# Optimization experiments

Measured on AMD Instinct MI355X. Metric: run time of the kernel, lower is better.

## Reference

```python
import jax, jax.numpy as jnp
import numpy as np

NOISE_STD = 0.001


def setup_inputs() -> dict:
    key = jax.random.key(0)
    k1, k2, k3, k4 = jax.random.split(key, 4)
    B, T, NIN, NREC = 64, 2048, 64, 1024
    x = jax.random.normal(k1, (B, T, NIN), dtype=jnp.float32)
    W_ih = jax.random.normal(k2, (NREC, NIN), dtype=jnp.float32) / np.sqrt(NIN)
    W_hh = jax.random.normal(k3, (NREC, NREC), dtype=jnp.float32) / np.sqrt(NREC)
    noise = jax.random.normal(k4, (T, NREC), dtype=jnp.float32)
    return {"x": x, "W_ih": W_ih, "W_hh": W_hh, "noise": noise}


def reference(x, W_ih, W_hh, noise):
    # x: [B, T, n_in] -> scan over time (strict sequential dependency)
    B = x.shape[0]
    NREC = W_hh.shape[0]
    x_t = jnp.transpose(x, (1, 0, 2))            # [T, B, n_in]
    xproj = jnp.einsum('tbi,ri->tbr', x_t, W_ih)  # hoist input GEMM out of scan
    noise_scaled = noise * NOISE_STD              # [T, NREC], broadcast over batch
    h0 = jnp.zeros((B, NREC), dtype=x.dtype)

    def step(h_prev, inp):
        xp, n_t = inp
        h = xp + jnp.tanh(h_prev) @ W_hh.T + n_t[None, :]
        return h, h[-1]  # original appends h_t[-1] (last batch element)

    h_last, outs = jax.lax.scan(step, h0, (xproj, noise_scaled))
    output = outs.T  # stack -> [T, NREC], transpose(0,1) -> [NREC, T]
    return output, h_last
```

## Files before the change

kernel.cpp:

```cpp
#include <hip/hip_runtime.h>


#define TT    2048
#define BB    64
#define NIN   64
#define NRECN 1024
#define KTOT  1088
#define MT    32
#define NT    32
#define NGRP  2
#define WPG   32
#define NWG   (NGRP * WPG)
#define NOISE_STD 0.001f

typedef __attribute__((ext_vector_type(8))) short short8;
typedef __attribute__((ext_vector_type(4))) float f32x4;

__device__ __forceinline__ unsigned short f2bf(float f) {
  unsigned u = __float_as_uint(f);
  u += 0x7FFFu + ((u >> 16) & 1u);
  return (unsigned short)(u >> 16);
}
__device__ __forceinline__ float bf2f(unsigned short h) {
  return __uint_as_float(((unsigned)h) << 16);
}
__device__ __forceinline__ void st_b16_sc1(unsigned short* p, unsigned short v) {
  unsigned vv = v;
  asm volatile("global_store_short %0, %1, off sc1" :: "v"(p), "v"(vv) : "memory");
}
__device__ __forceinline__ void split8(const f32x4& v0, const f32x4& v1,
                                       short8& ah, short8& al) {
  #pragma unroll
  for (int j = 0; j < 4; ++j) {
    unsigned short h = f2bf(v0[j]);
    ah[j] = (short)h; al[j] = (short)f2bf(v0[j] - bf2f(h));
  }
  #pragma unroll
  for (int j = 0; j < 4; ++j) {
    unsigned short h = f2bf(v1[j]);
    ah[4 + j] = (short)h; al[4 + j] = (short)f2bf(v1[j] - bf2f(h));
  }
}

#define LDA16(V, P, OFF) \
  asm volatile("global_load_dwordx4 %0, %1, off offset:%c2" \
               : "=&v"(V) : "v"(P), "n"(OFF))

__global__ __launch_bounds__(256, 1) void rnn_scan_kernel(
    const float* __restrict__ x, const float* __restrict__ W_ih,
    const float* __restrict__ W_hh, const float* __restrict__ noise,
    float* __restrict__ out, int* __restrict__ flags,
    unsigned short* __restrict__ th)
{
  extern __shared__ unsigned short smem[];
  unsigned short* w_hi = smem;
  unsigned short* w_lo = smem + KTOT * NT;

  const int wg = blockIdx.x, gm = wg / WPG, gn = wg % WPG;
  const int tid = threadIdx.x, lane = tid & 63, wv = tid >> 6;
  const int msub = wv >> 1, nsub = wv & 1;
  const int l15 = lane & 15, g4 = lane >> 4, lk8 = g4 * 8;

  for (int idx = tid; idx < NT * KTOT; idx += 256) {
    int nr = idx / KTOT, k = idx - nr * KTOT;
    int ng = gn * NT + nr;
    float v = (k < NRECN) ? W_hh[(size_t)ng * NRECN + k]
                          : W_ih[(size_t)ng * NIN + (k - NRECN)];
    unsigned short h = f2bf(v);
    unsigned short l = f2bf(v - bf2f(h));
    int widx = (k >> 3) * (NT * 8) + nr * 8 + (k & 7);
    w_hi[widx] = h; w_lo[widx] = l;
  }
  __syncthreads();

  int* flags_g = flags + gm * WPG * 16;
  const int mloc = msub * 16 + l15;
  const int nloc = nsub * 16 + l15;
  const int b_glob = gm * MT + mloc;
  const int n_glob = gn * NT + nloc;
  const unsigned short* whp = w_hi + g4 * 256 + nloc * 8;
  const unsigned short* wlp = w_lo + g4 * 256 + nloc * 8;
  const int grp_th = gm * (2 * WPG * MT * NT);
  const float* xrow = x + (size_t)b_glob * TT * NIN;

  f32x4 xv0, xv1, xv2, xv3;
  f32x4 xn0 = {0,0,0,0}, xn1 = {0,0,0,0}, xn2 = {0,0,0,0}, xn3 = {0,0,0,0};
  { const float* xp = xrow + lk8;
    xv0 = *(const f32x4*)xp;        xv1 = *(const f32x4*)(xp + 4);
    xv2 = *(const f32x4*)(xp + 32); xv3 = *(const f32x4*)(xp + 36); }
  float nzv = noise[n_glob] * NOISE_STD, nzn = 0.f;

  for (int t = 0; t < TT; ++t) {
    const int buf = t & 1;

    f32x4 p0 = {0,0,0,0}, p1 = {0,0,0,0}, q0 = {0,0,0,0}, q1 = {0,0,0,0};

    {
      short8 ah, al;
      split8(xv0, xv1, ah, al);
      short8 bh = *(const short8*)(whp + 32 * 1024);
      short8 bl = *(const short8*)(wlp + 32 * 1024);
      p0 = __builtin_amdgcn_mfma_f32_16x16x32_bf16(ah, bh, p0, 0, 0, 0);
      q0 = __builtin_amdgcn_mfma_f32_16x16x32_bf16(ah, bl, q0, 0, 0, 0);
      p1 = __builtin_amdgcn_mfma_f32_16x16x32_bf16(al, bh, p1, 0, 0, 0);
      split8(xv2, xv3, ah, al);
      bh = *(const short8*)(whp + 33 * 1024);
      bl = *(const short8*)(wlp + 33 * 1024);
      p1 = __builtin_amdgcn_mfma_f32_16x16x32_bf16(ah, bh, p1, 0, 0, 0);
      q1 = __builtin_amdgcn_mfma_f32_16x16x32_bf16(ah, bl, q1, 0, 0, 0);
      p0 = __builtin_amdgcn_mfma_f32_16x16x32_bf16(al, bh, p0, 0, 0, 0);
    }

    if (t > 0) {
      const int t4 = t << 2;
      if (lane < WPG) {
        while (__hip_atomic_load(&flags_g[lane * 16], __ATOMIC_RELAXED,
                                 __HIP_MEMORY_SCOPE_AGENT) < t4) { }
      }
      __builtin_amdgcn_fence(__ATOMIC_ACQUIRE, "agent");

      const unsigned short* abase =
          th + grp_th + buf * (WPG * MT * NT) + mloc * NT + lk8;
      const unsigned short* bp[16];
      #pragma unroll
      for (int j = 0; j < 16; ++j) bp[j] = abase + j * 2 * (MT * NT);
      short8 A[32];
      #pragma unroll
      for (int c = 0; c < 32; ++c)
        LDA16(A[c], bp[c >> 1], (c & 1) * (MT * NT * 2));
      asm volatile("s_waitcnt vmcnt(0)" ::: "memory");
      __builtin_amdgcn_sched_barrier(0);

      #pragma unroll
      for (int c = 0; c < 32; c += 2) {
        short8 b0h = *(const short8*)(whp + c * 1024);
        short8 b0l = *(const short8*)(wlp + c * 1024);
        p0 = __builtin_amdgcn_mfma_f32_16x16x32_bf16(A[c], b0h, p0, 0, 0, 0);
        q0 = __builtin_amdgcn_mfma_f32_16x16x32_bf16(A[c], b0l, q0, 0, 0, 0);
        short8 b1h = *(const short8*)(whp + (c + 1) * 1024);
        short8 b1l = *(const short8*)(wlp + (c + 1) * 1024);
        p1 = __builtin_amdgcn_mfma_f32_16x16x32_bf16(A[c+1], b1h, p1, 0, 0, 0);
        q1 = __builtin_amdgcn_mfma_f32_16x16x32_bf16(A[c+1], b1l, q1, 0, 0, 0);
      }
    }

    f32x4 hs = (p0 + p1) + (q0 + q1);
    const int nbuf = (t + 1) & 1;
    unsigned short* oh = th + grp_th + nbuf * (WPG * MT * NT) + gn * (MT * NT);
    float hout[4];
    #pragma unroll
    for (int r = 0; r < 4; ++r) {
      const int mr = msub * 16 + g4 * 4 + r;
      float h = hs[r] + nzv;
      hout[r] = h;
      float e  = __expf(2.f * h);
      float tv = 1.f - 2.f / (e + 1.f);
      st_b16_sc1(oh + mr * NT + nloc, f2bf(tv));
    }
    asm volatile("s_waitcnt vmcnt(0)" ::: "memory");
    if (lane == 0)
      __hip_atomic_fetch_add(&flags_g[gn * 16], 1, __ATOMIC_RELAXED,
                             __HIP_MEMORY_SCOPE_AGENT);

    #pragma unroll
    for (int r = 0; r < 4; ++r) {
      const int mr = msub * 16 + g4 * 4 + r;
      const int br = gm * MT + mr;
      if (br == BB - 1) out[(size_t)n_glob * TT + t] = hout[r];
      if (t == TT - 1)
        out[(size_t)NRECN * TT + (size_t)br * NRECN + n_glob] = hout[r];
    }
    if (t + 1 < TT) {
      const float* xp = xrow + (size_t)(t + 1) * NIN + lk8;
      xn0 = *(const f32x4*)xp;        xn1 = *(const f32x4*)(xp + 4);
      xn2 = *(const f32x4*)(xp + 32); xn3 = *(const f32x4*)(xp + 36);
      nzn = noise[(size_t)(t + 1) * NRECN + n_glob] * NOISE_STD;
    }
    xv0 = xn0; xv1 = xn1; xv2 = xn2; xv3 = xn3; nzv = nzn;
  }
}

extern "C" void kernel_launch(void* const* d_in, const int* in_sizes, int n_in,
                              void* d_out, int out_size, void* d_ws, size_t ws_size,
                              hipStream_t stream) {
  const float* x     = (const float*)d_in[0];
  const float* W_ih  = (const float*)d_in[1];
  const float* W_hh  = (const float*)d_in[2];
  const float* noise = (const float*)d_in[3];
  float* out = (float*)d_out;

  char* ws = (char*)d_ws;
  int* flags = (int*)ws;
  unsigned short* th = (unsigned short*)(ws + 4096);

  (void)hipMemsetAsync(flags, 0, 4096, stream);

  const size_t lds_bytes = (size_t)2 * KTOT * NT * sizeof(unsigned short);
  (void)hipFuncSetAttribute((const void*)rnn_scan_kernel,
                            hipFuncAttributeMaxDynamicSharedMemorySize,
                            (int)lds_bytes);

  rnn_scan_kernel<<<dim3(NWG), dim3(256), lds_bytes, stream>>>(
      x, W_ih, W_hh, noise, out, flags, th);
}
```

Before: 12.48 ms.

## Repartition RNN scan into 8 independent batch groups using fp16 weights

Recasts the persistent RNN scan so 128 workgroups form 8 groups of 16, each group handling 8 batch rows and each workgroup 64 output columns. Each group needs only 16 flags per step instead of 32, and the per-step state exchanged is smaller. The weights go from a bf16 hi/lo split to a single fp16 copy, which halves the weight MFMAs and LDS traffic, while the activations keep an fp16 hi/lo split. The tradeoffs are that 16x16 MFMA tiles are half wasted on 8 batch rows, the weight path loses precision, and the x/noise prefetch across steps is dropped.

```diff
diff --git a/kernel.cpp b/kernel.cpp
--- a/kernel.cpp
+++ b/kernel.cpp
@@ -6,39 +6,29 @@
 #define NIN   64
 #define NRECN 1024
 #define KTOT  1088
-#define MT    32
-#define NT    32
-#define NGRP  2
-#define WPG   32
-#define NWG   (NGRP * WPG)
+#define NGRP  8
+#define WPGRP 16
+#define NWG   128
 #define NOISE_STD 0.001f
 
-typedef __attribute__((ext_vector_type(8))) short short8;
+typedef __attribute__((ext_vector_type(8))) _Float16 half8;
 typedef __attribute__((ext_vector_type(4))) float f32x4;
 
-__device__ __forceinline__ unsigned short f2bf(float f) {
-  unsigned u = __float_as_uint(f);
-  u += 0x7FFFu + ((u >> 16) & 1u);
-  return (unsigned short)(u >> 16);
+__device__ __forceinline__ void st_h_sc1(_Float16* p, unsigned short u) {
+  unsigned v = u;
+  asm volatile("global_store_short %0, %1, off sc1" :: "v"(p), "v"(v) : "memory");
 }
-__device__ __forceinline__ float bf2f(unsigned short h) {
-  return __uint_as_float(((unsigned)h) << 16);
-}
-__device__ __forceinline__ void st_b16_sc1(unsigned short* p, unsigned short v) {
-  unsigned vv = v;
-  asm volatile("global_store_short %0, %1, off sc1" :: "v"(p), "v"(vv) : "memory");
-}
-__device__ __forceinline__ void split8(const f32x4& v0, const f32x4& v1,
-                                       short8& ah, short8& al) {
+__device__ __forceinline__ void split8h(const f32x4& v0, const f32x4& v1,
+                                        half8& hh, half8& hl) {
   #pragma unroll
   for (int j = 0; j < 4; ++j) {
-    unsigned short h = f2bf(v0[j]);
-    ah[j] = (short)h; al[j] = (short)f2bf(v0[j] - bf2f(h));
+    _Float16 h = (_Float16)v0[j];
+    hh[j] = h; hl[j] = (_Float16)(v0[j] - (float)h);
   }
   #pragma unroll
   for (int j = 0; j < 4; ++j) {
-    unsigned short h = f2bf(v1[j]);
-    ah[4 + j] = (short)h; al[4 + j] = (short)f2bf(v1[j] - bf2f(h));
+    _Float16 h = (_Float16)v1[j];
+    hh[4 + j] = h; hl[4 + j] = (_Float16)(v1[j] - (float)h);
   }
 }
 
@@ -46,137 +36,126 @@
   asm volatile("global_load_dwordx4 %0, %1, off offset:%c2" \
                : "=&v"(V) : "v"(P), "n"(OFF))
 
-__global__ __launch_bounds__(256, 1) void rnn_scan_kernel(
+#define MFMA16 __builtin_amdgcn_mfma_f32_16x16x32_f16
+
+__global__ __launch_bounds__(128, 1) void rnn_scan_kernel(
     const float* __restrict__ x, const float* __restrict__ W_ih,
     const float* __restrict__ W_hh, const float* __restrict__ noise,
     float* __restrict__ out, int* __restrict__ flags,
-    unsigned short* __restrict__ th)
+    _Float16* __restrict__ th)
 {
-  extern __shared__ unsigned short smem[];
-  unsigned short* w_hi = smem;
-  unsigned short* w_lo = smem + KTOT * NT;
+  extern __shared__ _Float16 smem[];
 
-  const int wg = blockIdx.x, gm = wg / WPG, gn = wg % WPG;
+  const int wg = blockIdx.x, grp = wg & 7, gidx = wg >> 3;
   const int tid = threadIdx.x, lane = tid & 63, wv = tid >> 6;
-  const int msub = wv >> 1, nsub = wv & 1;
-  const int l15 = lane & 15, g4 = lane >> 4, lk8 = g4 * 8;
+  const int l15 = lane & 15, g4 = lane >> 4;
 
-  for (int idx = tid; idx < NT * KTOT; idx += 256) {
+  for (int idx = tid; idx < 64 * KTOT; idx += 128) {
     int nr = idx / KTOT, k = idx - nr * KTOT;
-    int ng = gn * NT + nr;
+    int ng = gidx * 64 + nr;
     float v = (k < NRECN) ? W_hh[(size_t)ng * NRECN + k]
                           : W_ih[(size_t)ng * NIN + (k - NRECN)];
-    unsigned short h = f2bf(v);
-    unsigned short l = f2bf(v - bf2f(h));
-    int widx = (k >> 3) * (NT * 8) + nr * 8 + (k & 7);
-    w_hi[widx] = h; w_lo[widx] = l;
+    smem[(k >> 3) * 512 + nr * 8 + (k & 7)] = (_Float16)v;
   }
   __syncthreads();
 
-  int* flags_g = flags + gm * WPG * 16;
-  const int mloc = msub * 16 + l15;
-  const int nloc = nsub * 16 + l15;
-  const int b_glob = gm * MT + mloc;
-  const int n_glob = gn * NT + nloc;
-  const unsigned short* whp = w_hi + g4 * 256 + nloc * 8;
-  const unsigned short* wlp = w_lo + g4 * 256 + nloc * 8;
-  const int grp_th = gm * (2 * WPG * MT * NT);
-  const float* xrow = x + (size_t)b_glob * TT * NIN;
-
-  f32x4 xv0, xv1, xv2, xv3;
-  f32x4 xn0 = {0,0,0,0}, xn1 = {0,0,0,0}, xn2 = {0,0,0,0}, xn3 = {0,0,0,0};
-  { const float* xp = xrow + lk8;
-    xv0 = *(const f32x4*)xp;        xv1 = *(const f32x4*)(xp + 4);
-    xv2 = *(const f32x4*)(xp + 32); xv3 = *(const f32x4*)(xp + 36); }
-  float nzv = noise[n_glob] * NOISE_STD, nzn = 0.f;
+  int* flags_g = flags + grp * WPGRP * 16;
+  const _Float16* whp0 = smem + g4 * 512 + (wv * 32 + l15) * 8;
+  const _Float16* whp1 = whp0 + 128;
+  _Float16* thg = th + grp * (2 * 16 * 1024);
+  const int b_eff = grp * 8 + (l15 & 7);
+  const float* xrow = x + (size_t)b_eff * TT * NIN;
+  const int col0 = gidx * 64 + wv * 32 + l15, col1 = col0 + 16;
 
   for (int t = 0; t < TT; ++t) {
     const int buf = t & 1;
 
-    f32x4 p0 = {0,0,0,0}, p1 = {0,0,0,0}, q0 = {0,0,0,0}, q1 = {0,0,0,0};
+    const float* xp = xrow + (size_t)t * NIN + g4 * 8;
+    f32x4 v0 = *(const f32x4*)xp,        v1 = *(const f32x4*)(xp + 4);
+    f32x4 v2 = *(const f32x4*)(xp + 32), v3 = *(const f32x4*)(xp + 36);
+    const float nz0 = noise[(size_t)t * NRECN + col0] * NOISE_STD;
+    const float nz1 = noise[(size_t)t * NRECN + col1] * NOISE_STD;
 
+    f32x4 P0{0,0,0,0}, P1{0,0,0,0}, Q0{0,0,0,0}, Q1{0,0,0,0};
     {
-      short8 ah, al;
-      split8(xv0, xv1, ah, al);
-      short8 bh = *(const short8*)(whp + 32 * 1024);
-      short8 bl = *(const short8*)(wlp + 32 * 1024);
-      p0 = __builtin_amdgcn_mfma_f32_16x16x32_bf16(ah, bh, p0, 0, 0, 0);
-      q0 = __builtin_amdgcn_mfma_f32_16x16x32_bf16(ah, bl, q0, 0, 0, 0);
-      p1 = __builtin_amdgcn_mfma_f32_16x16x32_bf16(al, bh, p1, 0, 0, 0);
-      split8(xv2, xv3, ah, al);
-      bh = *(const short8*)(whp + 33 * 1024);
-      bl = *(const short8*)(wlp + 33 * 1024);
-      p1 = __builtin_amdgcn_mfma_f32_16x16x32_bf16(ah, bh, p1, 0, 0, 0);
-      q1 = __builtin_amdgcn_mfma_f32_16x16x32_bf16(ah, bl, q1, 0, 0, 0);
-      p0 = __builtin_amdgcn_mfma_f32_16x16x32_bf16(al, bh, p0, 0, 0, 0);
+      half8 xh, xl;
+      split8h(v0, v1, xh, xl);
+      half8 b0 = *(const half8*)(whp0 + 32 * 2048);
+      half8 b1 = *(const half8*)(whp1 + 32 * 2048);
+      P0 = MFMA16(xh, b0, P0, 0,0,0); P1 = MFMA16(xh, b1, P1, 0,0,0);
+      Q0 = MFMA16(xl, b0, Q0, 0,0,0); Q1 = MFMA16(xl, b1, Q1, 0,0,0);
+      split8h(v2, v3, xh, xl);
+      b0 = *(const half8*)(whp0 + 33 * 2048);
+      b1 = *(const half8*)(whp1 + 33 * 2048);
+      P0 = MFMA16(xh, b0, P0, 0,0,0); P1 = MFMA16(xh, b1, P1, 0,0,0);
+      Q0 = MFMA16(xl, b0, Q0, 0,0,0); Q1 = MFMA16(xl, b1, Q1, 0,0,0);
     }
 
     if (t > 0) {
-      const int t4 = t << 2;
-      if (lane < WPG) {
+      const int t2 = t << 1;
+      if (lane < WPGRP) {
         while (__hip_atomic_load(&flags_g[lane * 16], __ATOMIC_RELAXED,
-                                 __HIP_MEMORY_SCOPE_AGENT) < t4) { }
+                                 __HIP_MEMORY_SCOPE_AGENT) < t2) { }
       }
       __builtin_amdgcn_fence(__ATOMIC_ACQUIRE, "agent");
 
-      const unsigned short* abase =
-          th + grp_th + buf * (WPG * MT * NT) + mloc * NT + lk8;
-      const unsigned short* bp[16];
+      const _Float16* abase = thg + buf * 16384 + l15 * 1024 + g4 * 8;
+      half8 A[32];
       #pragma unroll
-      for (int j = 0; j < 16; ++j) bp[j] = abase + j * 2 * (MT * NT);
-      short8 A[32];
-      #pragma unroll
-      for (int c = 0; c < 32; ++c)
-        LDA16(A[c], bp[c >> 1], (c & 1) * (MT * NT * 2));
+      for (int c = 0; c < 32; ++c) LDA16(A[c], abase, c * 64);
       asm volatile("s_waitcnt vmcnt(0)" ::: "memory");
       __builtin_amdgcn_sched_barrier(0);
 
       #pragma unroll
       for (int c = 0; c < 32; c += 2) {
-        short8 b0h = *(const short8*)(whp + c * 1024);
-        short8 b0l = *(const short8*)(wlp + c * 1024);
-        p0 = __builtin_amdgcn_mfma_f32_16x16x32_bf16(A[c], b0h, p0, 0, 0, 0);
-        q0 = __builtin_amdgcn_mfma_f32_16x16x32_bf16(A[c], b0l, q0, 0, 0, 0);
-        short8 b1h = *(const short8*)(whp + (c + 1) * 1024);
-        short8 b1l = *(const short8*)(wlp + (c + 1) * 1024);
-        p1 = __builtin_amdgcn_mfma_f32_16x16x32_bf16(A[c+1], b1h, p1, 0, 0, 0);
-        q1 = __builtin_amdgcn_mfma_f32_16x16x32_bf16(A[c+1], b1l, q1, 0, 0, 0);
+        half8 e0 = *(const half8*)(whp0 + c * 2048);
+        half8 e1 = *(const half8*)(whp1 + c * 2048);
+        half8 o0 = *(const half8*)(whp0 + (c + 1) * 2048);
+        half8 o1 = *(const half8*)(whp1 + (c + 1) * 2048);
+        P0 = MFMA16(A[c],   e0, P0, 0,0,0); P1 = MFMA16(A[c],   e1, P1, 0,0,0);
+        Q0 = MFMA16(A[c+1], o0, Q0, 0,0,0); Q1 = MFMA16(A[c+1], o1, Q1, 0,0,0);
       }
     }
 
-    f32x4 hs = (p0 + p1) + (q0 + q1);
-    const int nbuf = (t + 1) & 1;
-    unsigned short* oh = th + grp_th + nbuf * (WPG * MT * NT) + gn * (MT * NT);
-    float hout[4];
+    f32x4 h0 = P0 + Q0, h1 = P1 + Q1;
+    _Float16* ob = thg + ((t + 1) & 1) * 16384;
+    float ho0[4], ho1[4];
     #pragma unroll
     for (int r = 0; r < 4; ++r) {
-      const int mr = msub * 16 + g4 * 4 + r;
-      float h = hs[r] + nzv;
-      hout[r] = h;
-      float e  = __expf(2.f * h);
-      float tv = 1.f - 2.f / (e + 1.f);
-      st_b16_sc1(oh + mr * NT + nloc, f2bf(tv));
+      const int mr = g4 * 4 + r;
+      float a0 = h0[r] + nz0, a1 = h1[r] + nz1;
+      ho0[r] = a0; ho1[r] = a1;
+      if (mr < 8) {
+        float t0 = 1.f - 2.f / (__expf(2.f * a0) + 1.f);
+        float t1 = 1.f - 2.f / (__expf(2.f * a1) + 1.f);
+        st_h_sc1(ob + mr * 1024 + col0,
+                 __builtin_bit_cast(unsigned short, (_Float16)t0));
+        st_h_sc1(ob + mr * 1024 + col1,
+                 __builtin_bit_cast(unsigned short, (_Float16)t1));
+      }
     }
     asm volatile("s_waitcnt vmcnt(0)" ::: "memory");
     if (lane == 0)
-      __hip_atomic_fetch_add(&flags_g[gn * 16], 1, __ATOMIC_RELAXED,
+      __hip_atomic_fetch_add(&flags_g[gidx * 16], 1, __ATOMIC_RELAXED,
                              __HIP_MEMORY_SCOPE_AGENT);
 
-    #pragma unroll
-    for (int r = 0; r < 4; ++r) {
-      const int mr = msub * 16 + g4 * 4 + r;
-      const int br = gm * MT + mr;
-      if (br == BB - 1) out[(size_t)n_glob * TT + t] = hout[r];
-      if (t == TT - 1)
-        out[(size_t)NRECN * TT + (size_t)br * NRECN + n_glob] = hout[r];
+    if (grp == NGRP - 1 || t == TT - 1) {
+      #pragma unroll
+      for (int r = 0; r < 4; ++r) {
+        const int mr = g4 * 4 + r;
+        if (mr < 8) {
+          const int br = grp * 8 + mr;
+          if (br == BB - 1) {
+            out[(size_t)col0 * TT + t] = ho0[r];
+            out[(size_t)col1 * TT + t] = ho1[r];
+          }
+          if (t == TT - 1) {
+            out[(size_t)NRECN * TT + (size_t)br * NRECN + col0] = ho0[r];
+            out[(size_t)NRECN * TT + (size_t)br * NRECN + col1] = ho1[r];
+          }
+        }
+      }
     }
-    if (t + 1 < TT) {
-      const float* xp = xrow + (size_t)(t + 1) * NIN + lk8;
-      xn0 = *(const f32x4*)xp;        xn1 = *(const f32x4*)(xp + 4);
-      xn2 = *(const f32x4*)(xp + 32); xn3 = *(const f32x4*)(xp + 36);
-      nzn = noise[(size_t)(t + 1) * NRECN + n_glob] * NOISE_STD;
-    }
-    xv0 = xn0; xv1 = xn1; xv2 = xn2; xv3 = xn3; nzv = nzn;
   }
 }
 
@@ -191,15 +170,15 @@
 
   char* ws = (char*)d_ws;
   int* flags = (int*)ws;
-  unsigned short* th = (unsigned short*)(ws + 4096);
+  _Float16* th = (_Float16*)(ws + 8192);
 
-  (void)hipMemsetAsync(flags, 0, 4096, stream);
+  (void)hipMemsetAsync(flags, 0, 8192, stream);
 
-  const size_t lds_bytes = (size_t)2 * KTOT * NT * sizeof(unsigned short);
+  const size_t lds_bytes = (size_t)136 * 64 * 8 * sizeof(_Float16);
   (void)hipFuncSetAttribute((const void*)rnn_scan_kernel,
                             hipFuncAttributeMaxDynamicSharedMemorySize,
                             (int)lds_bytes);
 
-  rnn_scan_kernel<<<dim3(NWG), dim3(256), lds_bytes, stream>>>(
+  rnn_scan_kernel<<<dim3(NWG), dim3(128), lds_bytes, stream>>>(
       x, W_ih, W_hh, noise, out, flags, th);
 }
```

Result: slower. 12.80 ms (+2.6%).
